# Optimization experiments

Measured on AMD Instinct MI355X. Metric: run time of the kernel, lower is better.

Reference implementation:

```python
import jax, jax.numpy as jnp
import numpy as np

N_NODES = 50000
N_EDGES = 800000
IN_DIM = 128
HID_DIM = 128
OUT_DIM = 64


def _sage_conv(x, edge_index, W_l, b_l, W_r):
    # PyG SAGEConv(aggr='mean'): out = lin_l(mean_agg(x_src -> dst)) + lin_r(x)
    src = edge_index[0]
    dst = edge_index[1]
    msgs = x[src]  # [E, D] gather
    summed = jax.ops.segment_sum(msgs, dst, num_segments=N_NODES)  # [N, D]
    cnt = jax.ops.segment_sum(jnp.ones((msgs.shape[0],), x.dtype), dst, num_segments=N_NODES)
    mean = summed / jnp.maximum(cnt, 1.0)[:, None]
    return mean @ W_l.T + b_l + x @ W_r.T


def setup_inputs() -> dict:
    key = jax.random.key(0)
    ks = jax.random.split(key, 9)
    x = jax.random.normal(ks[0], (N_NODES, IN_DIM), dtype=jnp.float32)
    edge_index = jax.random.randint(ks[1], (2, N_EDGES), 0, N_NODES, dtype=jnp.int64)

    def glorot(k, shape):
        lim = float(np.sqrt(6.0 / (shape[0] + shape[1])))
        return jax.random.uniform(k, shape, dtype=jnp.float32, minval=-lim, maxval=lim)

    W1_l = glorot(ks[2], (HID_DIM, IN_DIM))
    b1_l = jnp.zeros((HID_DIM,), jnp.float32)
    W1_r = glorot(ks[3], (HID_DIM, IN_DIM))
    W2_l = glorot(ks[4], (HID_DIM, HID_DIM))
    b2_l = jnp.zeros((HID_DIM,), jnp.float32)
    W2_r = glorot(ks[5], (HID_DIM, HID_DIM))
    W3 = glorot(ks[6], (OUT_DIM, HID_DIM))
    b3 = jnp.zeros((OUT_DIM,), jnp.float32)
    return {"x": x, "edge_index": edge_index,
            "W1_l": W1_l, "b1_l": b1_l, "W1_r": W1_r,
            "W2_l": W2_l, "b2_l": b2_l, "W2_r": W2_r,
            "W3": W3, "b3": b3}


def reference(x, edge_index, W1_l, b1_l, W1_r, W2_l, b2_l, W2_r, W3, b3):
    h = _sage_conv(x, edge_index, W1_l, b1_l, W1_r)
    h = jax.nn.relu(h)
    # dropout is identity in eval mode
    h = _sage_conv(h, edge_index, W2_l, b2_l, W2_r)
    h = jax.nn.relu(h)
    out = h @ W3.T + b3
    return jax.nn.relu(out)
```

## Files before the change

kernel.cpp:

```cpp
#include <hip/hip_runtime.h>
#include <hip/hip_bf16.h>

#define N_NODES 50000
#define N_EDGES 800000
#define NBUCK 391
#define CAP 4096

typedef short bf16x8 __attribute__((ext_vector_type(8)));
typedef float f32x4 __attribute__((ext_vector_type(4)));
typedef float floatx2 __attribute__((ext_vector_type(2)));

__device__ inline unsigned short f2b(float f) {
    union { float f; unsigned u; } v; v.f = f;
    unsigned r = v.u + 0x7FFF + ((v.u >> 16) & 1);
    return (unsigned short)(r >> 16);
}
__device__ inline float b2f(unsigned short u) {
    union { unsigned u; float f; } v; v.u = ((unsigned)u) << 16; return v.f;
}

#define XITEMS 1600000
#define WITEMS 18432
#define PB_EDGES 4096
#define SCAT_BLKS 196

__global__ __launch_bounds__(512) void prep_scatter(
        const float* __restrict__ x, unsigned short* __restrict__ xb,
        unsigned char* __restrict__ x8,
        const float* __restrict__ W1l, const float* __restrict__ W1r,
        const float* __restrict__ W2l, const float* __restrict__ W2r,
        const float* __restrict__ W3,
        unsigned short* __restrict__ w1lb, unsigned short* __restrict__ w1rb,
        unsigned short* __restrict__ w2lb, unsigned short* __restrict__ w2rb,
        unsigned short* __restrict__ w3b,
        const int* __restrict__ ei, int* __restrict__ bucketCount,
        unsigned long long* __restrict__ pairBuf) {
    __shared__ int hist[NBUCK];
    __shared__ int gbase[NBUCK];
    const int t = threadIdx.x;

    if (blockIdx.x < SCAT_BLKS) {
        const int E = N_EDGES;
        for (int i = t; i < NBUCK; i += 512) hist[i] = 0;
        __syncthreads();
        const int base = blockIdx.x * PB_EDGES;
        int srcv[8], dstv[8], lr[8], bk[8];
#pragma unroll
        for (int j = 0; j < 8; ++j) {
            int idx = base + j * 512 + t;
            if (idx < E) {
                srcv[j] = ei[idx];
                dstv[j] = ei[E + idx];
                bk[j] = dstv[j] >> 7;
                lr[j] = atomicAdd(&hist[bk[j]], 1);
            } else {
                bk[j] = -1; srcv[j] = 0; dstv[j] = 0; lr[j] = 0;
            }
        }
        __syncthreads();
        for (int i = t; i < NBUCK; i += 512) {
            int h = hist[i];
            if (h) gbase[i] = i * CAP + atomicAdd(&bucketCount[i], h);
        }
        __syncthreads();
#pragma unroll
        for (int j = 0; j < 8; ++j) {
            if (bk[j] >= 0) {
                int pos = gbase[bk[j]] + lr[j];
                pairBuf[pos] = ((unsigned long long)(unsigned)dstv[j] << 32) | (unsigned)srcv[j];
            }
        }
        return;
    }

    int gid = (blockIdx.x - SCAT_BLKS) * 512 + t;
    if (gid < XITEMS) {
        int idx = gid * 4;
        float4 v = *reinterpret_cast<const float4*>(x + idx);
        ushort4 o;
        o.x = f2b(v.x); o.y = f2b(v.y); o.z = f2b(v.z); o.w = f2b(v.w);
        *reinterpret_cast<ushort4*>(xb + idx) = o;
        unsigned r = __builtin_amdgcn_cvt_pk_fp8_f32(v.x, v.y, 0, false);
        r = __builtin_amdgcn_cvt_pk_fp8_f32(v.z, v.w, r, true);
        *reinterpret_cast<unsigned*>(x8 + idx) = r;
        return;
    }
    gid -= XITEMS;
    if (gid < WITEMS) {
        int idx = gid * 4;
        const float* s; unsigned short* o; int base;
        if      (idx < 16384) { s = W1l; o = w1lb; base = 0; }
        else if (idx < 32768) { s = W1r; o = w1rb; base = 16384; }
        else if (idx < 49152) { s = W2l; o = w2lb; base = 32768; }
        else if (idx < 65536) { s = W2r; o = w2rb; base = 49152; }
        else                  { s = W3;  o = w3b;  base = 65536; }
        int k = idx - base;
        float4 v = *reinterpret_cast<const float4*>(s + k);
        ushort4 w;
        w.x = f2b(v.x); w.y = f2b(v.y); w.z = f2b(v.z); w.w = f2b(v.w);
        *reinterpret_cast<ushort4*>(o + k) = w;
    }
}

__global__ __launch_bounds__(512) void csr_sort(
        const unsigned long long* __restrict__ pairBuf,
        const int* __restrict__ bucketCount,
        int* __restrict__ offs, int* __restrict__ csr, int n) {
    __shared__ int sm[512];
    __shared__ int nb[128];
    __shared__ int nc[128];
    const int b = blockIdx.x, t = threadIdx.x;
    int v = (t < NBUCK) ? bucketCount[t] : 0;
    sm[t] = v;
    __syncthreads();
    for (int o = 1; o < 512; o <<= 1) {
        int a = (t >= o) ? sm[t - o] : 0;
        __syncthreads();
        sm[t] += a;
        __syncthreads();
    }
    const int count = bucketCount[b];
    const int base = sm[b] - count;
    const int node0 = b << 7;
    const int nN = min(128, n - node0);
    if (t < 128) nc[t] = 0;
    __syncthreads();
    const unsigned long long* pb = pairBuf + (size_t)b * CAP;
    for (int i = t; i < count; i += 512) {
        int d = ((int)(pb[i] >> 32)) & 127;
        atomicAdd(&nc[d], 1);
    }
    __syncthreads();
    if (t < 128) sm[t] = nc[t];
    __syncthreads();
    for (int o = 1; o < 128; o <<= 1) {
        int a = 0;
        if (t < 128 && t >= o) a = sm[t - o];
        __syncthreads();
        if (t < 128) sm[t] += a;
        __syncthreads();
    }
    if (t < 128) nb[t] = base + sm[t] - nc[t];
    __syncthreads();
    if (t < nN) offs[node0 + t] = nb[t];
    if (b == NBUCK - 1 && t == 0) offs[n] = base + count;
    if (t < 128) nc[t] = 0;
    __syncthreads();
    for (int i = t; i < count; i += 512) {
        unsigned long long p = pb[i];
        int d = ((int)(p >> 32)) & 127;
        int r = atomicAdd(&nc[d], 1);
        csr[nb[d] + r] = (int)(p & 0xffffffffu);
    }
}

__global__ __launch_bounds__(256) void cvt8(const unsigned short* __restrict__ src,
                                            unsigned char* __restrict__ dst, int n) {
    int idx = (blockIdx.x * 256 + threadIdx.x) * 8;
    if (idx >= n) return;
    uint4 v = *reinterpret_cast<const uint4*>(src + idx);
    float f0 = b2f((unsigned short)(v.x & 0xffff)), f1 = b2f((unsigned short)(v.x >> 16));
    float f2 = b2f((unsigned short)(v.y & 0xffff)), f3 = b2f((unsigned short)(v.y >> 16));
    float f4 = b2f((unsigned short)(v.z & 0xffff)), f5 = b2f((unsigned short)(v.z >> 16));
    float f6 = b2f((unsigned short)(v.w & 0xffff)), f7 = b2f((unsigned short)(v.w >> 16));
    uint2 o;
    o.x = __builtin_amdgcn_cvt_pk_fp8_f32(f0, f1, 0, false);
    o.x = __builtin_amdgcn_cvt_pk_fp8_f32(f2, f3, o.x, true);
    o.y = __builtin_amdgcn_cvt_pk_fp8_f32(f4, f5, 0, false);
    o.y = __builtin_amdgcn_cvt_pk_fp8_f32(f6, f7, o.y, true);
    *reinterpret_cast<uint2*>(dst + idx) = o;
}

__device__ inline void acc8f(float* a, uint2 v) {
    floatx2 p;
    p = __builtin_amdgcn_cvt_pk_f32_fp8(v.x, false); a[0] += p.x; a[1] += p.y;
    p = __builtin_amdgcn_cvt_pk_f32_fp8(v.x, true);  a[2] += p.x; a[3] += p.y;
    p = __builtin_amdgcn_cvt_pk_f32_fp8(v.y, false); a[4] += p.x; a[5] += p.y;
    p = __builtin_amdgcn_cvt_pk_f32_fp8(v.y, true);  a[6] += p.x; a[7] += p.y;
}

__global__ __launch_bounds__(256, 8) void aggregate_fp8(
        const unsigned char* __restrict__ feat8, const int* __restrict__ offs,
        const int* __restrict__ csr, unsigned short* __restrict__ out, int n) {
    int grp = (blockIdx.x * 256 + threadIdx.x) >> 4;
    int l = threadIdx.x & 15;
    if (grp >= n) return;
    int beg = offs[grp], end = offs[grp + 1];
    int deg = end - beg;
    float acc[8] = {};
    for (int cb = 0; cb < deg; cb += 16) {
        int rem = deg - cb; if (rem > 16) rem = 16;
        int e = (cb + l < deg) ? csr[beg + cb + l] : 0;
        int j = 0;
        for (; j + 7 < rem; j += 8) {
            uint2 v[8];
#pragma unroll
            for (int k = 0; k < 8; ++k) {
                int s = __shfl(e, j + k, 16);
                v[k] = *reinterpret_cast<const uint2*>(feat8 + (size_t)s * 128 + l * 8);
            }
#pragma unroll
            for (int k = 0; k < 8; ++k) acc8f(acc, v[k]);
        }
        for (; j < rem; ++j) {
            int s = __shfl(e, j, 16);
            uint2 v = *reinterpret_cast<const uint2*>(feat8 + (size_t)s * 128 + l * 8);
            acc8f(acc, v);
        }
    }
    float inv = deg > 0 ? 1.f / (float)deg : 0.f;
    uint4 o;
    o.x = (unsigned)f2b(acc[0] * inv) | ((unsigned)f2b(acc[1] * inv) << 16);
    o.y = (unsigned)f2b(acc[2] * inv) | ((unsigned)f2b(acc[3] * inv) << 16);
    o.z = (unsigned)f2b(acc[4] * inv) | ((unsigned)f2b(acc[5] * inv) << 16);
    o.w = (unsigned)f2b(acc[6] * inv) | ((unsigned)f2b(acc[7] * inv) << 16);
    *reinterpret_cast<uint4*>(out + (size_t)grp * 128 + l * 8) = o;
}

__global__ __launch_bounds__(256, 8) void gemm_layer(
        const unsigned short* __restrict__ A1, const unsigned short* __restrict__ B1,
        const unsigned short* __restrict__ A2, const unsigned short* __restrict__ B2,
        const float* __restrict__ bias, unsigned short* __restrict__ C, int M) {
    constexpr int K = 128;
    const int lane = threadIdx.x & 63;
    const int wv = threadIdx.x >> 6;
    const int wrow = (wv & 1) * 16;
    const int ch = wv >> 1;
    const int rowBase = blockIdx.x * 32 + wrow;
    const int fr = lane & 15;
    const int fq = lane >> 4;

    f32x4 acc[4];
#pragma unroll
    for (int j = 0; j < 4; ++j) acc[j] = (f32x4){0.f, 0.f, 0.f, 0.f};

#pragma unroll
    for (int pass = 0; pass < 2; ++pass) {
        const unsigned short* A = pass ? A2 : A1;
        const unsigned short* B = pass ? B2 : B1;
        bf16x8 af[4];
        {
            int r = rowBase + fr;
            r = r < M ? r : M - 1;
            const unsigned short* p = A + (size_t)r * K + fq * 8;
#pragma unroll
            for (int ks = 0; ks < 4; ++ks)
                af[ks] = *reinterpret_cast<const bf16x8*>(p + ks * 32);
        }
#pragma unroll
        for (int nt = 0; nt < 4; ++nt) {
            const unsigned short* q = B + (size_t)(ch * 64 + nt * 16 + fr) * K + fq * 8;
#pragma unroll
            for (int ks = 0; ks < 4; ++ks) {
                bf16x8 bfr = *reinterpret_cast<const bf16x8*>(q + ks * 32);
                acc[nt] = __builtin_amdgcn_mfma_f32_16x16x32_bf16(af[ks], bfr, acc[nt], 0, 0, 0);
            }
        }
    }

#pragma unroll
    for (int i = 0; i < 4; ++i) {
        int gm = rowBase + fq * 4 + i;
        if (gm >= M) continue;
#pragma unroll
        for (int nt = 0; nt < 4; ++nt) {
            int c = ch * 64 + nt * 16 + fr;
            float v = acc[nt][i] + bias[c];
            C[(size_t)gm * 128 + c] = f2b(v > 0.f ? v : 0.f);
        }
    }
}

__global__ __launch_bounds__(256, 8) void gemm2_head(
        const unsigned short* __restrict__ A1, const unsigned short* __restrict__ B1,
        const unsigned short* __restrict__ A2, const unsigned short* __restrict__ B2,
        const float* __restrict__ bias,
        const unsigned short* __restrict__ W3, const float* __restrict__ b3,
        float* __restrict__ out, int M) {
    __shared__ char lds[32 * 256];
    constexpr int K = 128;
    const int lane = threadIdx.x & 63;
    const int wv = threadIdx.x >> 6;
    const int wrow = (wv & 1) * 16;
    const int ch = wv >> 1;
    const int rowBase = blockIdx.x * 32 + wrow;
    const int fr = lane & 15;
    const int fq = lane >> 4;

    f32x4 acc[4];
#pragma unroll
    for (int j = 0; j < 4; ++j) acc[j] = (f32x4){0.f, 0.f, 0.f, 0.f};

#pragma unroll
    for (int pass = 0; pass < 2; ++pass) {
        const unsigned short* A = pass ? A2 : A1;
        const unsigned short* B = pass ? B2 : B1;
        bf16x8 af[4];
        {
            int r = rowBase + fr;
            r = r < M ? r : M - 1;
            const unsigned short* p = A + (size_t)r * K + fq * 8;
#pragma unroll
            for (int ks = 0; ks < 4; ++ks)
                af[ks] = *reinterpret_cast<const bf16x8*>(p + ks * 32);
        }
#pragma unroll
        for (int nt = 0; nt < 4; ++nt) {
            const unsigned short* q = B + (size_t)(ch * 64 + nt * 16 + fr) * K + fq * 8;
#pragma unroll
            for (int ks = 0; ks < 4; ++ks) {
                bf16x8 bfr = *reinterpret_cast<const bf16x8*>(q + ks * 32);
                acc[nt] = __builtin_amdgcn_mfma_f32_16x16x32_bf16(af[ks], bfr, acc[nt], 0, 0, 0);
            }
        }
    }

#pragma unroll
    for (int i = 0; i < 4; ++i) {
        int rL = wrow + fq * 4 + i;
#pragma unroll
        for (int nt = 0; nt < 4; ++nt) {
            int c = ch * 64 + nt * 16 + fr;
            float v = acc[nt][i] + bias[c];
            int off = (rL * 256 + c * 2) ^ ((rL & 7) << 4);
            *reinterpret_cast<unsigned short*>(lds + off) = f2b(v > 0.f ? v : 0.f);
        }
    }
    __syncthreads();

    f32x4 acc3[2];
#pragma unroll
    for (int j = 0; j < 2; ++j) acc3[j] = (f32x4){0.f, 0.f, 0.f, 0.f};
    const int rl = wrow + fr;
    bf16x8 a3[4];
#pragma unroll
    for (int ks = 0; ks < 4; ++ks) {
        int off = (rl * 256 + ks * 64 + fq * 16) ^ ((rl & 7) << 4);
        a3[ks] = *reinterpret_cast<const bf16x8*>(lds + off);
    }
#pragma unroll
    for (int nt = 0; nt < 2; ++nt) {
        int wcol = ch * 32 + nt * 16 + fr;
        const unsigned short* q = W3 + (size_t)wcol * K + fq * 8;
#pragma unroll
        for (int ks = 0; ks < 4; ++ks) {
            bf16x8 bw = *reinterpret_cast<const bf16x8*>(q + ks * 32);
            acc3[nt] = __builtin_amdgcn_mfma_f32_16x16x32_bf16(a3[ks], bw, acc3[nt], 0, 0, 0);
        }
    }
#pragma unroll
    for (int i = 0; i < 4; ++i) {
        int gm = rowBase + fq * 4 + i;
        if (gm >= M) continue;
#pragma unroll
        for (int nt = 0; nt < 2; ++nt) {
            int c = ch * 32 + nt * 16 + fr;
            float v = acc3[nt][i] + b3[c];
            out[(size_t)gm * 64 + c] = v > 0.f ? v : 0.f;
        }
    }
}

extern "C" void kernel_launch(void* const* d_in, const int* in_sizes, int n_in,
                              void* d_out, int out_size, void* d_ws, size_t ws_size,
                              hipStream_t stream) {
    const float* x   = (const float*)d_in[0];
    const int*   ei  = (const int*)d_in[1];
    const float* W1l = (const float*)d_in[2];
    const float* b1l = (const float*)d_in[3];
    const float* W1r = (const float*)d_in[4];
    const float* W2l = (const float*)d_in[5];
    const float* b2l = (const float*)d_in[6];
    const float* W2r = (const float*)d_in[7];
    const float* W3  = (const float*)d_in[8];
    const float* b3  = (const float*)d_in[9];
    float* out = (float*)d_out;

    const int NN = N_NODES, E = N_EDGES;

    char* base = (char*)d_ws;
    unsigned short* xb    = (unsigned short*)(base + 0);
    unsigned short* h1b   = (unsigned short*)(base + 12800000);
    unsigned short* meanb = (unsigned short*)(base + 25600000);
    unsigned char*  x8    = (unsigned char*) (base + 38400000);
    unsigned char*  h18   = (unsigned char*) (base + 44800000);
    unsigned short* w1lb  = (unsigned short*)(base + 51200000);
    unsigned short* w1rb  = (unsigned short*)(base + 51232768);
    unsigned short* w2lb  = (unsigned short*)(base + 51265536);
    unsigned short* w2rb  = (unsigned short*)(base + 51298304);
    unsigned short* w3b   = (unsigned short*)(base + 51331072);
    int* offs             = (int*)(base + 51347456);
    int* bucketCount      = (int*)(base + 51547520);
    int* csr              = (int*)(base + 51549120);
    unsigned long long* pairBuf = (unsigned long long*)(base + 54749184);

    hipMemsetAsync(bucketCount, 0, 1600, stream);

    const int PREP_BLKS = (XITEMS + WITEMS + 511) / 512;
    prep_scatter<<<SCAT_BLKS + PREP_BLKS, 512, 0, stream>>>(
        x, xb, x8, W1l, W1r, W2l, W2r, W3, w1lb, w1rb, w2lb, w2rb, w3b,
        ei, bucketCount, pairBuf);

    csr_sort<<<NBUCK, 512, 0, stream>>>(pairBuf, bucketCount, offs, csr, NN);

    const int AGG_BLK = (NN * 16 + 255) / 256;
    const int GB32 = (NN + 31) / 32;

    aggregate_fp8<<<AGG_BLK, 256, 0, stream>>>(x8, offs, csr, meanb, NN);
    gemm_layer<<<GB32, 256, 0, stream>>>(meanb, w1lb, xb, w1rb, b1l, h1b, NN);
    cvt8<<<(NN * 128 / 8 + 255) / 256, 256, 0, stream>>>(h1b, h18, NN * 128);

    aggregate_fp8<<<AGG_BLK, 256, 0, stream>>>(h18, offs, csr, meanb, NN);
    gemm2_head<<<GB32, 256, 0, stream>>>(meanb, w2lb, h1b, w2rb, b2l, w3b, b3, out, NN);
}
```

Measured before the change: 155.1 us.

## Restructure SAGE GEMMs into 64-row tiles with register-resident weights and LDS-staged activations

The two layer GEMM kernels merge into one templated kernel that processes 64 rows per block. Each wave loads its slice of both weight matrices, plus W3 for the head, into registers once and reuses them across two 16-row subtiles. Activation rows are staged through swizzled LDS with coalesced loads instead of being read directly from global memory. Workspace buffers are padded to N_PAD so the unguarded 64-row loads past M stay in bounds, at the cost of higher register and LDS use (launch bounds drop to 2 blocks per SM).

```diff
diff --git a/kernel.cpp b/kernel.cpp
--- a/kernel.cpp
+++ b/kernel.cpp
@@ -2,6 +2,7 @@
 #include <hip/hip_bf16.h>
 
 #define N_NODES 50000
+#define N_PAD 50048
 #define N_EDGES 800000
 #define NBUCK 391
 #define CAP 4096
@@ -217,146 +218,142 @@
     *reinterpret_cast<uint4*>(out + (size_t)grp * 128 + l * 8) = o;
 }
 
-__global__ __launch_bounds__(256, 8) void gemm_layer(
-        const unsigned short* __restrict__ A1, const unsigned short* __restrict__ B1,
-        const unsigned short* __restrict__ A2, const unsigned short* __restrict__ B2,
-        const float* __restrict__ bias, unsigned short* __restrict__ C, int M) {
-    constexpr int K = 128;
-    const int lane = threadIdx.x & 63;
-    const int wv = threadIdx.x >> 6;
-    const int wrow = (wv & 1) * 16;
-    const int ch = wv >> 1;
-    const int rowBase = blockIdx.x * 32 + wrow;
-    const int fr = lane & 15;
-    const int fq = lane >> 4;
-
-    f32x4 acc[4];
-#pragma unroll
-    for (int j = 0; j < 4; ++j) acc[j] = (f32x4){0.f, 0.f, 0.f, 0.f};
-
-#pragma unroll
-    for (int pass = 0; pass < 2; ++pass) {
-        const unsigned short* A = pass ? A2 : A1;
-        const unsigned short* B = pass ? B2 : B1;
-        bf16x8 af[4];
-        {
-            int r = rowBase + fr;
-            r = r < M ? r : M - 1;
-            const unsigned short* p = A + (size_t)r * K + fq * 8;
-#pragma unroll
-            for (int ks = 0; ks < 4; ++ks)
-                af[ks] = *reinterpret_cast<const bf16x8*>(p + ks * 32);
-        }
-#pragma unroll
-        for (int nt = 0; nt < 4; ++nt) {
-            const unsigned short* q = B + (size_t)(ch * 64 + nt * 16 + fr) * K + fq * 8;
-#pragma unroll
-            for (int ks = 0; ks < 4; ++ks) {
-                bf16x8 bfr = *reinterpret_cast<const bf16x8*>(q + ks * 32);
-                acc[nt] = __builtin_amdgcn_mfma_f32_16x16x32_bf16(af[ks], bfr, acc[nt], 0, 0, 0);
-            }
-        }
-    }
-
-#pragma unroll
-    for (int i = 0; i < 4; ++i) {
-        int gm = rowBase + fq * 4 + i;
-        if (gm >= M) continue;
-#pragma unroll
-        for (int nt = 0; nt < 4; ++nt) {
-            int c = ch * 64 + nt * 16 + fr;
-            float v = acc[nt][i] + bias[c];
-            C[(size_t)gm * 128 + c] = f2b(v > 0.f ? v : 0.f);
-        }
-    }
-}
-
-__global__ __launch_bounds__(256, 8) void gemm2_head(
+template<bool HEAD>
+__global__ __launch_bounds__(256, 2) void gemm_k(
         const unsigned short* __restrict__ A1, const unsigned short* __restrict__ B1,
         const unsigned short* __restrict__ A2, const unsigned short* __restrict__ B2,
         const float* __restrict__ bias,
         const unsigned short* __restrict__ W3, const float* __restrict__ b3,
-        float* __restrict__ out, int M) {
-    __shared__ char lds[32 * 256];
-    constexpr int K = 128;
-    const int lane = threadIdx.x & 63;
-    const int wv = threadIdx.x >> 6;
-    const int wrow = (wv & 1) * 16;
-    const int ch = wv >> 1;
-    const int rowBase = blockIdx.x * 32 + wrow;
-    const int fr = lane & 15;
-    const int fq = lane >> 4;
-
-    f32x4 acc[4];
-#pragma unroll
-    for (int j = 0; j < 4; ++j) acc[j] = (f32x4){0.f, 0.f, 0.f, 0.f};
-
-#pragma unroll
-    for (int pass = 0; pass < 2; ++pass) {
-        const unsigned short* A = pass ? A2 : A1;
-        const unsigned short* B = pass ? B2 : B1;
-        bf16x8 af[4];
-        {
-            int r = rowBase + fr;
-            r = r < M ? r : M - 1;
-            const unsigned short* p = A + (size_t)r * K + fq * 8;
+        void* __restrict__ outP, int M) {
+    __shared__ char lds[HEAD ? 49152 : 32768];
+    const int t = threadIdx.x;
+    const int rowBase = blockIdx.x * 64;
+    const int lane = t & 63, wv = t >> 6;
+    const int ch = wv & 1, half = wv >> 1;
+    const int fr = lane & 15, fq = lane >> 4;
+    const int swz = (fr & 7) << 4;
+
+    const char* a1p = (const char*)(A1 + (size_t)rowBase * 128);
+    const char* a2p = (const char*)(A2 + (size_t)rowBase * 128);
+    uint4 st[8];
+#pragma unroll
+    for (int c = 0; c < 4; ++c) {
+        int q = c * 4096 + t * 16;
+        int src = q ^ (((q >> 8) & 7) << 4);
+        st[c]     = *reinterpret_cast<const uint4*>(a1p + src);
+        st[4 + c] = *reinterpret_cast<const uint4*>(a2p + src);
+    }
+
+    bf16x8 bl[4][4], br[4][4];
+#pragma unroll
+    for (int nt = 0; nt < 4; ++nt) {
+        const unsigned short* ql = B1 + (size_t)(ch * 64 + nt * 16 + fr) * 128 + fq * 8;
+        const unsigned short* qr = B2 + (size_t)(ch * 64 + nt * 16 + fr) * 128 + fq * 8;
+#pragma unroll
+        for (int ks = 0; ks < 4; ++ks) {
+            bl[nt][ks] = *reinterpret_cast<const bf16x8*>(ql + ks * 32);
+            br[nt][ks] = *reinterpret_cast<const bf16x8*>(qr + ks * 32);
+        }
+    }
+    bf16x8 w3f[2][4];
+    if (HEAD) {
+#pragma unroll
+        for (int nt = 0; nt < 2; ++nt) {
+            const unsigned short* q = W3 + (size_t)(ch * 32 + nt * 16 + fr) * 128 + fq * 8;
 #pragma unroll
             for (int ks = 0; ks < 4; ++ks)
-                af[ks] = *reinterpret_cast<const bf16x8*>(p + ks * 32);
-        }
-#pragma unroll
-        for (int nt = 0; nt < 4; ++nt) {
-            const unsigned short* q = B + (size_t)(ch * 64 + nt * 16 + fr) * K + fq * 8;
+                w3f[nt][ks] = *reinterpret_cast<const bf16x8*>(q + ks * 32);
+        }
+    }
+
+#pragma unroll
+    for (int c = 0; c < 4; ++c) {
+        *reinterpret_cast<uint4*>(lds + c * 4096 + t * 16)         = st[c];
+        *reinterpret_cast<uint4*>(lds + 16384 + c * 4096 + t * 16) = st[4 + c];
+    }
+    __syncthreads();
+
+#pragma unroll
+    for (int tt = 0; tt < 2; ++tt) {
+        const int rl = half * 32 + tt * 16 + fr;
+        const int rb = rl * 256;
+        f32x4 acc[4];
+#pragma unroll
+        for (int j = 0; j < 4; ++j) acc[j] = (f32x4){0.f, 0.f, 0.f, 0.f};
+        bf16x8 a1[4], a2[4];
+#pragma unroll
+        for (int ks = 0; ks < 4; ++ks) {
+            int off = rb + fq * 16 + ks * 64;
+            a1[ks] = *reinterpret_cast<const bf16x8*>(lds + (off ^ swz));
+            a2[ks] = *reinterpret_cast<const bf16x8*>(lds + 16384 + (off ^ swz));
+        }
+#pragma unroll
+        for (int nt = 0; nt < 4; ++nt)
 #pragma unroll
             for (int ks = 0; ks < 4; ++ks) {
-                bf16x8 bfr = *reinterpret_cast<const bf16x8*>(q + ks * 32);
-                acc[nt] = __builtin_amdgcn_mfma_f32_16x16x32_bf16(af[ks], bfr, acc[nt], 0, 0, 0);
-            }
-        }
-    }
-
-#pragma unroll
-    for (int i = 0; i < 4; ++i) {
-        int rL = wrow + fq * 4 + i;
-#pragma unroll
-        for (int nt = 0; nt < 4; ++nt) {
-            int c = ch * 64 + nt * 16 + fr;
-            float v = acc[nt][i] + bias[c];
-            int off = (rL * 256 + c * 2) ^ ((rL & 7) << 4);
-            *reinterpret_cast<unsigned short*>(lds + off) = f2b(v > 0.f ? v : 0.f);
-        }
-    }
-    __syncthreads();
-
-    f32x4 acc3[2];
-#pragma unroll
-    for (int j = 0; j < 2; ++j) acc3[j] = (f32x4){0.f, 0.f, 0.f, 0.f};
-    const int rl = wrow + fr;
-    bf16x8 a3[4];
-#pragma unroll
-    for (int ks = 0; ks < 4; ++ks) {
-        int off = (rl * 256 + ks * 64 + fq * 16) ^ ((rl & 7) << 4);
-        a3[ks] = *reinterpret_cast<const bf16x8*>(lds + off);
-    }
-#pragma unroll
-    for (int nt = 0; nt < 2; ++nt) {
-        int wcol = ch * 32 + nt * 16 + fr;
-        const unsigned short* q = W3 + (size_t)wcol * K + fq * 8;
-#pragma unroll
-        for (int ks = 0; ks < 4; ++ks) {
-            bf16x8 bw = *reinterpret_cast<const bf16x8*>(q + ks * 32);
-            acc3[nt] = __builtin_amdgcn_mfma_f32_16x16x32_bf16(a3[ks], bw, acc3[nt], 0, 0, 0);
-        }
-    }
-#pragma unroll
-    for (int i = 0; i < 4; ++i) {
-        int gm = rowBase + fq * 4 + i;
-        if (gm >= M) continue;
-#pragma unroll
-        for (int nt = 0; nt < 2; ++nt) {
-            int c = ch * 32 + nt * 16 + fr;
-            float v = acc3[nt][i] + b3[c];
-            out[(size_t)gm * 64 + c] = v > 0.f ? v : 0.f;
+                acc[nt] = __builtin_amdgcn_mfma_f32_16x16x32_bf16(a1[ks], bl[nt][ks], acc[nt], 0, 0, 0);
+                acc[nt] = __builtin_amdgcn_mfma_f32_16x16x32_bf16(a2[ks], br[nt][ks], acc[nt], 0, 0, 0);
+            }
+        if (!HEAD) {
+            unsigned short* C = (unsigned short*)outP;
+#pragma unroll
+            for (int i = 0; i < 4; ++i) {
+                int gm = rowBase + half * 32 + tt * 16 + fq * 4 + i;
+                if (gm >= M) continue;
+#pragma unroll
+                for (int nt = 0; nt < 4; ++nt) {
+                    int c = ch * 64 + nt * 16 + fr;
+                    float v = acc[nt][i] + bias[c];
+                    C[(size_t)gm * 128 + c] = f2b(v > 0.f ? v : 0.f);
+                }
+            }
+        } else {
+#pragma unroll
+            for (int i = 0; i < 4; ++i) {
+                int rL = half * 32 + tt * 16 + fq * 4 + i;
+#pragma unroll
+                for (int nt = 0; nt < 4; ++nt) {
+                    int c = ch * 64 + nt * 16 + fr;
+                    float v = acc[nt][i] + bias[c];
+                    int off = (rL * 256 + c * 2) ^ ((rL & 7) << 4);
+                    *reinterpret_cast<unsigned short*>(lds + 32768 + off) = f2b(v > 0.f ? v : 0.f);
+                }
+            }
+        }
+    }
+
+    if (HEAD) {
+        __syncthreads();
+        float* out = (float*)outP;
+#pragma unroll
+        for (int tt = 0; tt < 2; ++tt) {
+            const int rl = half * 32 + tt * 16 + fr;
+            const int rb = rl * 256;
+            bf16x8 a3[4];
+#pragma unroll
+            for (int ks = 0; ks < 4; ++ks) {
+                int off = rb + fq * 16 + ks * 64;
+                a3[ks] = *reinterpret_cast<const bf16x8*>(lds + 32768 + (off ^ swz));
+            }
+            f32x4 acc3[2];
+#pragma unroll
+            for (int j = 0; j < 2; ++j) acc3[j] = (f32x4){0.f, 0.f, 0.f, 0.f};
+#pragma unroll
+            for (int nt = 0; nt < 2; ++nt)
+#pragma unroll
+                for (int ks = 0; ks < 4; ++ks)
+                    acc3[nt] = __builtin_amdgcn_mfma_f32_16x16x32_bf16(a3[ks], w3f[nt][ks], acc3[nt], 0, 0, 0);
+#pragma unroll
+            for (int i = 0; i < 4; ++i) {
+                int gm = rowBase + half * 32 + tt * 16 + fq * 4 + i;
+                if (gm >= M) continue;
+#pragma unroll
+                for (int nt = 0; nt < 2; ++nt) {
+                    int c = ch * 32 + nt * 16 + fr;
+                    float v = acc3[nt][i] + b3[c];
+                    out[(size_t)gm * 64 + c] = v > 0.f ? v : 0.f;
+                }
+            }
         }
     }
 }
@@ -380,19 +377,19 @@
 
     char* base = (char*)d_ws;
     unsigned short* xb    = (unsigned short*)(base + 0);
-    unsigned short* h1b   = (unsigned short*)(base + 12800000);
-    unsigned short* meanb = (unsigned short*)(base + 25600000);
-    unsigned char*  x8    = (unsigned char*) (base + 38400000);
-    unsigned char*  h18   = (unsigned char*) (base + 44800000);
-    unsigned short* w1lb  = (unsigned short*)(base + 51200000);
-    unsigned short* w1rb  = (unsigned short*)(base + 51232768);
-    unsigned short* w2lb  = (unsigned short*)(base + 51265536);
-    unsigned short* w2rb  = (unsigned short*)(base + 51298304);
-    unsigned short* w3b   = (unsigned short*)(base + 51331072);
-    int* offs             = (int*)(base + 51347456);
-    int* bucketCount      = (int*)(base + 51547520);
-    int* csr              = (int*)(base + 51549120);
-    unsigned long long* pairBuf = (unsigned long long*)(base + 54749184);
+    unsigned short* h1b   = (unsigned short*)(base + 12812288);
+    unsigned short* meanb = (unsigned short*)(base + 25624576);
+    unsigned char*  x8    = (unsigned char*) (base + 38436864);
+    unsigned char*  h18   = (unsigned char*) (base + 44836864);
+    unsigned short* w1lb  = (unsigned short*)(base + 51236864);
+    unsigned short* w1rb  = (unsigned short*)(base + 51269632);
+    unsigned short* w2lb  = (unsigned short*)(base + 51302400);
+    unsigned short* w2rb  = (unsigned short*)(base + 51335168);
+    unsigned short* w3b   = (unsigned short*)(base + 51367936);
+    int* offs             = (int*)(base + 51384320);
+    int* bucketCount      = (int*)(base + 51584384);
+    int* csr              = (int*)(base + 51586048);
+    unsigned long long* pairBuf = (unsigned long long*)(base + 54786048);
 
     hipMemsetAsync(bucketCount, 0, 1600, stream);
 
@@ -404,12 +401,14 @@
     csr_sort<<<NBUCK, 512, 0, stream>>>(pairBuf, bucketCount, offs, csr, NN);
 
     const int AGG_BLK = (NN * 16 + 255) / 256;
-    const int GB32 = (NN + 31) / 32;
+    const int GB64 = (NN + 63) / 64;
 
     aggregate_fp8<<<AGG_BLK, 256, 0, stream>>>(x8, offs, csr, meanb, NN);
-    gemm_layer<<<GB32, 256, 0, stream>>>(meanb, w1lb, xb, w1rb, b1l, h1b, NN);
+    gemm_k<false><<<GB64, 256, 0, stream>>>(meanb, w1lb, xb, w1rb, b1l,
+                                            nullptr, nullptr, h1b, NN);
     cvt8<<<(NN * 128 / 8 + 255) / 256, 256, 0, stream>>>(h1b, h18, NN * 128);
 
     aggregate_fp8<<<AGG_BLK, 256, 0, stream>>>(h18, offs, csr, meanb, NN);
-    gemm2_head<<<GB32, 256, 0, stream>>>(meanb, w2lb, h1b, w2rb, b2l, w3b, b3, out, NN);
-}
+    gemm_k<true><<<GB64, 256, 0, stream>>>(meanb, w2lb, h1b, w2rb, b2l,
+                                           w3b, b3, out, NN);
+}
```

Result: faster. 128.7 us (-17.0%).
